# Optimization experiments

Hardware: AMD Instinct MI355X
Metric: run time of the kernel (lower is better)

## Reference

```python
import jax, jax.numpy as jnp
import numpy as np

HEADS, DQK, DV = 4, 128, 128
HH, WW = 32, 32
SCALE = DQK ** -0.5
EPS = 1e-5


def bn(x, g, b, m, v):
    # eval-mode BatchNorm2d over channel dim of NCHW
    inv = g * jax.lax.rsqrt(v + EPS)
    return x * inv[:, None, None] + (b - m * inv)[:, None, None]


def rel_to_abs(x):
    # x: (B, Nh, L, 2L-1) -> (B, Nh, L, L)
    B, Nh, L, _ = x.shape
    x = jnp.pad(x, ((0, 0), (0, 0), (0, 0), (0, 1)))
    fx = x.reshape(B, Nh, L * 2 * L)
    fx = jnp.pad(fx, ((0, 0), (0, 0), (0, L - 1)))
    fx = fx.reshape(B, Nh, L + 1, 2 * L - 1)
    return fx[:, :, :L, L - 1:]


def rel_logits_1d(q, rel_k):
    # q: (B, Nh, H, W, D); rel_k: (2W-1, D)
    B, Nh, H, W, D = q.shape
    r = jnp.einsum('bnhwd,rd->bnhwr', q, rel_k)
    r = rel_to_abs(r.reshape(B, Nh * H, W, 2 * W - 1))
    r = r.reshape(B, Nh, H, W, W)
    return jnp.broadcast_to(r[:, :, :, None], (B, Nh, H, H, W, W))


def pos_bias(q, rel_h, rel_w):
    # q: (B, Nh, H*W, D), already scaled
    B, Nh, L, D = q.shape
    q5 = q.reshape(B, Nh, HH, WW, D)
    rw = rel_logits_1d(q5, rel_w)                     # (B,N,H,Hx,W,W)
    rw = rw.transpose(0, 1, 2, 4, 3, 5).reshape(B, Nh, HH * WW, HH * WW)
    rh = rel_logits_1d(q5.transpose(0, 1, 3, 2, 4), rel_h)  # (B,N,W,Wx,H,H)
    rh = rh.transpose(0, 1, 4, 2, 5, 3).reshape(B, Nh, HH * WW, HH * WW)
    return rw + rh


def to_heads(x):
    # (B, Nh*d, H, W) -> (B, Nh, H*W, d)
    B, C, H, W = x.shape
    x = x.reshape(B, HEADS, C // HEADS, H, W)
    return x.transpose(0, 1, 3, 4, 2).reshape(B, HEADS, H * W, C // HEADS)


def mhsa(x, w_qk, w_v, rel_h, rel_w):
    B, C, H, W = x.shape
    qk = jnp.einsum('bchw,oc->bohw', x, w_qk)
    q, k = jnp.split(qk, 2, axis=1)
    v = jnp.einsum('bchw,oc->bohw', x, w_v)
    q, k, v = to_heads(q), to_heads(k), to_heads(v)
    q = q * SCALE
    logits = jnp.einsum('bnid,bnjd->bnij', q, k) + pos_bias(q, rel_h, rel_w)
    weights = jax.nn.softmax(logits, axis=-1)
    out = jnp.einsum('bnij,bnjd->bnid', weights, v)   # (B,Nh,HW,dv)
    out = out.reshape(B, HEADS, H, W, DV).transpose(0, 1, 4, 2, 3)
    return out.reshape(B, HEADS * DV, H, W)


def setup_inputs() -> dict:
    key = jax.random.key(0)
    ks = jax.random.split(key, 12)
    d = {
        'x': jax.random.normal(ks[0], (8, 512, HH, WW), jnp.float32),
        'w_qk': jax.random.normal(ks[1], (2 * HEADS * DQK, 512), jnp.float32) * 0.02,
        'w_v': jax.random.normal(ks[2], (HEADS * DV, 512), jnp.float32) * 0.02,
        'rel_h': jax.random.normal(ks[3], (2 * HH - 1, DQK), jnp.float32) * SCALE,
        'rel_w': jax.random.normal(ks[4], (2 * WW - 1, DQK), jnp.float32) * SCALE,
        'g1': jnp.ones((512,), jnp.float32),
        'b1': jnp.zeros((512,), jnp.float32),
        'm1': jax.random.normal(ks[5], (512,), jnp.float32) * 0.1,
        'v1': jax.random.uniform(ks[6], (512,), jnp.float32) + 0.5,
        'g2': jnp.ones((512,), jnp.float32),
        'b2': jnp.zeros((512,), jnp.float32),
        'm2': jax.random.normal(ks[7], (512,), jnp.float32) * 0.1,
        'v2': jax.random.uniform(ks[8], (512,), jnp.float32) + 0.5,
        'w_fc': jax.random.normal(ks[9], (512, 512, 3, 3), jnp.float32) * 0.02,
        'bias_fc': jnp.zeros((512,), jnp.float32),
    }
    return d


def reference(x, w_qk, w_v, rel_h, rel_w, g1, b1, m1, v1, g2, b2, m2, v2, w_fc, bias_fc):
    out = jax.nn.relu(bn(x, g1, b1, m1, v1))
    out = mhsa(out, w_qk, w_v, rel_h, rel_w)
    x = out + x
    out = jax.nn.relu(bn(x, g2, b2, m2, v2))
    out = jax.lax.conv_general_dilated(
        out, w_fc, window_strides=(1, 1), padding='SAME',
        dimension_numbers=('NCHW', 'OIHW', 'NCHW')) + bias_fc[:, None, None]
    return out + x
```

## Files before the change

kernel.cpp:

```cpp
#include <hip/hip_runtime.h>

typedef __bf16 v8bf __attribute__((ext_vector_type(8)));
typedef float f32x4 __attribute__((ext_vector_type(4)));

#define DEVI static __device__ __forceinline__

DEVI v8bf load8(const __bf16* p) { return *reinterpret_cast<const v8bf*>(p); }

DEVI f32x4 mfma16(v8bf a, v8bf b, f32x4 c) {
  return __builtin_amdgcn_mfma_f32_16x16x32_bf16(a, b, c, 0, 0, 0);
}

DEVI void gld16(const __bf16* g, __bf16* l) {
  __builtin_amdgcn_global_load_lds(
      (const __attribute__((address_space(1))) unsigned int*)(const void*)g,
      (__attribute__((address_space(3))) unsigned int*)(void*)l, 16, 0, 0);
}

#define SCALE_Q 0.08838834764831845f

__global__ void k_prep(const float* __restrict__ wqk, const float* __restrict__ wv,
                       const float* __restrict__ relh, const float* __restrict__ relw,
                       const float* __restrict__ wfc, __bf16* __restrict__ wqkb,
                       __bf16* __restrict__ wvb, __bf16* __restrict__ rhb,
                       __bf16* __restrict__ rwb, __bf16* __restrict__ Wt,
                       float* __restrict__ zpad4) {
  const int bid = blockIdx.x, tid = threadIdx.x;
  if (bid < 2048) {
    int i = bid * 256 + tid;
    wqkb[i] = (__bf16)wqk[i];
  } else if (bid < 3072) {
    int i = (bid - 2048) * 256 + tid;
    wvb[i] = (__bf16)wv[i];
  } else if (bid < 3104) {
    int i = (bid - 3072) * 256 + tid;
    if (i < 8064) rhb[i] = (__bf16)relh[i];
  } else if (bid < 3136) {
    int i = (bid - 3104) * 256 + tid;
    if (i < 8064) rwb[i] = (__bf16)relw[i];
  } else if (bid < 4160) {
    int i = (bid - 3136) * 256 + tid;
    const float* src = wfc + (size_t)i * 9;
#pragma unroll
    for (int tap = 0; tap < 9; ++tap)
      Wt[(size_t)tap * 262144 + i] = (__bf16)src[tap];
  } else {
    int i = (bid - 4160) * 256 + tid;
    f32x4 z = {0.f, 0.f, 0.f, 0.f};
    reinterpret_cast<f32x4*>(zpad4)[i] = z;
  }
}

__global__ void k_bn1(const float* __restrict__ x, const float* __restrict__ g,
                      const float* __restrict__ bb, const float* __restrict__ m,
                      const float* __restrict__ v, __bf16* __restrict__ y) {
  __shared__ float tile[32][33];
  const int b = blockIdx.z, c0 = blockIdx.y * 32, s0 = blockIdx.x * 32;
  const int tx = threadIdx.x, ty = threadIdx.y;
#pragma unroll
  for (int r = 0; r < 4; ++r) {
    int c = c0 + ty + r * 8;
    float inv = g[c] * rsqrtf(v[c] + 1e-5f);
    float beta = bb[c] - m[c] * inv;
    float val = x[((size_t)b * 512 + c) * 1024 + s0 + tx] * inv + beta;
    tile[ty + r * 8][tx] = fmaxf(val, 0.0f);
  }
  __syncthreads();
#pragma unroll
  for (int r = 0; r < 4; ++r) {
    int s = s0 + ty + r * 8;
    y[((size_t)b * 1024 + s) * 512 + c0 + tx] = (__bf16)tile[tx][ty + r * 8];
  }
}

__global__ void k_bn2(const float* __restrict__ x2, const float* __restrict__ g,
                      const float* __restrict__ bb, const float* __restrict__ m,
                      const float* __restrict__ v, __bf16* __restrict__ zp) {
  __shared__ float tile[32][33];
  const int b = blockIdx.z, c0 = blockIdx.y * 32, s0 = blockIdx.x * 32;
  const int tx = threadIdx.x, ty = threadIdx.y;
#pragma unroll
  for (int r = 0; r < 4; ++r) {
    int c = c0 + ty + r * 8;
    float inv = g[c] * rsqrtf(v[c] + 1e-5f);
    float beta = bb[c] - m[c] * inv;
    float val = x2[((size_t)b * 512 + c) * 1024 + s0 + tx] * inv + beta;
    tile[ty + r * 8][tx] = fmaxf(val, 0.0f);
  }
  __syncthreads();
#pragma unroll
  for (int r = 0; r < 4; ++r) {
    int s = s0 + ty + r * 8;
    int hh = s >> 5, ww = s & 31;
    zp[(((size_t)b * 34 + hh + 1) * 34 + ww + 1) * 512 + c0 + tx] =
        (__bf16)tile[tx][ty + r * 8];
  }
}

__global__ __launch_bounds__(256) void k_proj(
    const __bf16* __restrict__ wall, const __bf16* __restrict__ y,
    __bf16* __restrict__ qout, __bf16* __restrict__ kout,
    __bf16* __restrict__ vout) {
  __shared__ __bf16 As[128 * 32];
  __shared__ __bf16 Bs[128 * 32];
  const int t = threadIdx.x;
  const int wave = t >> 6, lane = t & 63;
  const int l15 = lane & 15, quad = lane >> 4;
  const int mbase = blockIdx.x * 128;
  const int nbase = blockIdx.y * 128;
  const int mh = (wave >> 1) * 64, nh = (wave & 1) * 64;
  const bool isv = mbase >= 1024;

  const int row0 = t >> 2, part8 = (t & 3) * 8;
  const __bf16* gA0 = wall + (size_t)(mbase + row0) * 512 + part8;
  const __bf16* gA1 = gA0 + (size_t)64 * 512;
  const __bf16* gB0 = y + (size_t)(nbase + row0) * 512 + part8;
  const __bf16* gB1 = gB0 + (size_t)64 * 512;
  __bf16* lA0 = As + (size_t)(wave * 64) * 8;
  __bf16* lA1 = As + (size_t)(256 + wave * 64) * 8;
  __bf16* lB0 = Bs + (size_t)(wave * 64) * 8;
  __bf16* lB1 = Bs + (size_t)(256 + wave * 64) * 8;

  const f32x4 fz = {0.f, 0.f, 0.f, 0.f};
  f32x4 acc[4][4];
#pragma unroll
  for (int i = 0; i < 4; ++i)
#pragma unroll
    for (int j = 0; j < 4; ++j) acc[i][j] = fz;

  for (int k0 = 0; k0 < 512; k0 += 32) {
    __syncthreads();
    gld16(gA0 + k0, lA0);
    gld16(gA1 + k0, lA1);
    gld16(gB0 + k0, lB0);
    gld16(gB1 + k0, lB1);
    __syncthreads();
    v8bf a[4], bfr[4];
#pragma unroll
    for (int i = 0; i < 4; ++i)
      a[i] = load8(&As[(size_t)(mh + i * 16 + l15) * 32 + quad * 8]);
#pragma unroll
    for (int j = 0; j < 4; ++j)
      bfr[j] = load8(&Bs[(size_t)(nh + j * 16 + l15) * 32 + quad * 8]);
    if (isv) {
#pragma unroll
      for (int i = 0; i < 4; ++i)
#pragma unroll
        for (int j = 0; j < 4; ++j) acc[i][j] = mfma16(a[i], bfr[j], acc[i][j]);
    } else {
#pragma unroll
      for (int i = 0; i < 4; ++i)
#pragma unroll
        for (int j = 0; j < 4; ++j) acc[i][j] = mfma16(bfr[j], a[i], acc[i][j]);
    }
  }

  if (isv) {
#pragma unroll
    for (int i = 0; i < 4; ++i)
#pragma unroll
      for (int j = 0; j < 4; ++j)
#pragma unroll
        for (int r = 0; r < 4; ++r) {
          int o = mbase + mh + i * 16 + quad * 4 + r;
          int nflat = nbase + nh + j * 16 + l15;
          int b = nflat >> 10, s = nflat & 1023;
          int oe = o - 1024; int n = oe >> 7, d = oe & 127;
          vout[(((size_t)b * 4 + n) * 128 + d) * 1024 + s] = (__bf16)acc[i][j][r];
        }
  } else {
    const bool isq = mbase < 512;
#pragma unroll
    for (int i = 0; i < 4; ++i)
#pragma unroll
      for (int j = 0; j < 4; ++j)
#pragma unroll
        for (int r = 0; r < 4; ++r) {
          int o = mbase + mh + i * 16 + l15;
          int nflat = nbase + nh + j * 16 + quad * 4 + r;
          int b = nflat >> 10, s = nflat & 1023;
          float val = acc[i][j][r];
          if (isq) {
            int n = o >> 7, d = o & 127;
            qout[(((size_t)b * 4 + n) * 1024 + s) * 128 + d] = (__bf16)(val * SCALE_Q);
          } else {
            int oe = o - 512; int n = oe >> 7, d = oe & 127;
            kout[(((size_t)b * 4 + n) * 1024 + s) * 128 + d] = (__bf16)val;
          }
        }
  }
}

__global__ __launch_bounds__(256, 2) void k_attn(
    const __bf16* __restrict__ q, const __bf16* __restrict__ kmat,
    const __bf16* __restrict__ vt, const __bf16* __restrict__ relh,
    const __bf16* __restrict__ relw, const float* __restrict__ x,
    float* __restrict__ x2) {
  __shared__ __bf16 Ks[2][4 * 64 * 32];
  __shared__ __bf16 Vs[2 * 128 * 32];
  __shared__ __bf16 P[4 * 16 * 68];
  __shared__ __bf16 RWs[64][33];
  __shared__ __bf16 RHs[64][33];
  __shared__ float Lt[4][16];

  const int Lb = blockIdx.x;
  const int xcd = Lb & 7, local = Lb >> 3;
  const int bn = xcd * 4 + (local & 3);
  const int qblk = local >> 2;
  const int s0 = qblk * 64;

  const int t = threadIdx.x;
  const int wave = t >> 6, lane = t & 63;
  const int l15 = lane & 15, quad = lane >> 4;
  const size_t hoff = ((size_t)bn) << 17;
  const int s0w = s0 + wave * 16;
  const int wlo = (wave & 1) * 16;
  const int h0w = s0w >> 5;

  const int row0 = t >> 2, part8 = (t & 3) * 8;
  const __bf16* kg = kmat + hoff + (size_t)row0 * 128 + part8;
  const __bf16* vg = vt + hoff + (size_t)row0 * 1024 + part8;
  __bf16* vsw = Vs + wave * 512;
  __bf16* ksw0 = Ks[0] + wave * 512;
  __bf16* ksw1 = Ks[1] + wave * 512;

#pragma unroll
  for (int kk2 = 0; kk2 < 2; ++kk2)
#pragma unroll
    for (int dh = 0; dh < 2; ++dh)
      gld16(vg + (size_t)dh * 64 * 1024 + kk2 * 32, vsw + kk2 * 4096 + dh * 2048);
#pragma unroll
  for (int kk = 0; kk < 4; ++kk)
    gld16(kg + kk * 32, ksw0 + kk * 2048);

  v8bf aq[4];
  {
    const __bf16* qp = q + hoff + (size_t)(s0w + l15) * 128;
#pragma unroll
    for (int kk = 0; kk < 4; ++kk) aq[kk] = load8(qp + kk * 32 + quad * 8);
  }

#pragma unroll
  for (int nt = 0; nt < 4; ++nt) {
    int rr = nt * 16 + l15;
    const __bf16* bp = relw + (size_t)rr * 128;
    f32x4 acc = {0.f, 0.f, 0.f, 0.f};
#pragma unroll
    for (int kk = 0; kk < 4; ++kk)
      acc = mfma16(aq[kk], load8(bp + kk * 32 + quad * 8), acc);
#pragma unroll
    for (int r = 0; r < 4; ++r) {
      int row = quad * 4 + r;
      int wj = rr + wlo + row - 31;
      if (wj >= 0 && wj < 32) RWs[wave * 16 + row][wj] = (__bf16)acc[r];
    }
  }
#pragma unroll
  for (int nt = 0; nt < 2; ++nt) {
    int hj = nt * 16 + l15;
    const __bf16* bp = relh + (size_t)(hj - h0w + 31) * 128;
    f32x4 acc = {0.f, 0.f, 0.f, 0.f};
#pragma unroll
    for (int kk = 0; kk < 4; ++kk)
      acc = mfma16(aq[kk], load8(bp + kk * 32 + quad * 8), acc);
#pragma unroll
    for (int r = 0; r < 4; ++r) RHs[wave * 16 + quad * 4 + r][hj] = (__bf16)acc[r];
  }

  __syncthreads();

  float rwreg[4][2];
#pragma unroll
  for (int r = 0; r < 4; ++r) {
    const int gi = wave * 16 + quad * 4 + r;
    rwreg[r][0] = (float)RWs[gi][l15];
    rwreg[r][1] = (float)RWs[gi][l15 + 16];
  }

  const f32x4 fz = {0.f, 0.f, 0.f, 0.f};
  float lsum[4] = {0.f, 0.f, 0.f, 0.f};
  f32x4 oacc[8];
#pragma unroll
  for (int dt = 0; dt < 8; ++dt) oacc[dt] = fz;
  __bf16* Pw = P + wave * 16 * 68;

#pragma unroll 1
  for (int iter = 0; iter < 16; ++iter) {
    const int cur = iter & 1;
    const __bf16* kcur = Ks[cur];
    __bf16* knxt = cur ? ksw0 : ksw1;
    const int jp = (iter < 15 ? iter + 1 : 15) * 64;

#pragma unroll
    for (int kk = 0; kk < 4; ++kk)
      gld16(kg + (size_t)jp * 128 + kk * 32, knxt + kk * 2048);

    f32x4 sacc[4];
    __builtin_amdgcn_s_setprio(1);
#pragma unroll
    for (int nj = 0; nj < 4; ++nj) {
      f32x4 a = fz;
#pragma unroll
      for (int kk = 0; kk < 4; ++kk)
        a = mfma16(aq[kk],
                   load8(&kcur[kk * 2048 + (nj * 16 + l15) * 32 + quad * 8]), a);
      sacc[nj] = a;
    }
    __builtin_amdgcn_s_setprio(0);

    const int hjb = iter * 2;
#pragma unroll
    for (int r = 0; r < 4; ++r) {
      const int row = quad * 4 + r;
      const int gi = wave * 16 + row;
      const float rw0 = rwreg[r][0], rw1 = rwreg[r][1];
      const float rh0 = (float)RHs[gi][hjb], rh1 = (float)RHs[gi][hjb + 1];
#pragma unroll
      for (int nj = 0; nj < 4; ++nj) {
        float val = sacc[nj][r] + ((nj & 1) ? rw1 : rw0) + ((nj & 2) ? rh1 : rh0);
        float p = __expf(fminf(val, 60.0f));
        lsum[r] += p;
        Pw[row * 68 + nj * 16 + l15] = (__bf16)p;
      }
    }
    v8bf pf[2];
#pragma unroll
    for (int kk2 = 0; kk2 < 2; ++kk2)
      pf[kk2] = *reinterpret_cast<const v8bf*>(&Pw[l15 * 68 + kk2 * 32 + quad * 8]);

    asm volatile("s_waitcnt vmcnt(4)" ::: "memory");
    __builtin_amdgcn_s_barrier();
    __builtin_amdgcn_sched_barrier(0);

    __builtin_amdgcn_s_setprio(1);
#pragma unroll
    for (int dt = 0; dt < 8; ++dt) {
      f32x4 a = oacc[dt];
#pragma unroll
      for (int kk2 = 0; kk2 < 2; ++kk2)
        a = mfma16(load8(&Vs[kk2 * 4096 + (dt * 16 + l15) * 32 + quad * 8]),
                   pf[kk2], a);
      oacc[dt] = a;
    }
    __builtin_amdgcn_s_setprio(0);

    __syncthreads();

#pragma unroll
    for (int kk2 = 0; kk2 < 2; ++kk2)
#pragma unroll
      for (int dh = 0; dh < 2; ++dh)
        gld16(vg + (size_t)dh * 64 * 1024 + jp + kk2 * 32,
              vsw + kk2 * 4096 + dh * 2048);
  }

#pragma unroll
  for (int r = 0; r < 4; ++r)
#pragma unroll
    for (int msk = 8; msk >= 1; msk >>= 1) lsum[r] += __shfl_xor(lsum[r], msk);
  if (l15 == 0) {
#pragma unroll
    for (int r = 0; r < 4; ++r) Lt[wave][quad * 4 + r] = lsum[r];
  }
  __syncthreads();

  {
    const float linv = 1.0f / Lt[wave][l15];
    const int s = s0w + l15;
#pragma unroll
    for (int dt = 0; dt < 8; ++dt)
#pragma unroll
      for (int r = 0; r < 4; ++r) {
        int d = dt * 16 + quad * 4 + r;
        size_t idx = ((size_t)bn * 128 + d) * 1024 + s;
        x2[idx] = oacc[dt][r] * linv + x[idx];
      }
  }
}

__global__ __launch_bounds__(256, 2) void k_conv(
    const __bf16* __restrict__ Wt, const __bf16* __restrict__ zp,
    float* __restrict__ part) {
  __shared__ __bf16 As[4 * 128 * 32];
  __shared__ __bf16 Bs[4 * 128 * 32];
  const int t = threadIdx.x;
  const int wave = t >> 6, lane = t & 63;
  const int l15 = lane & 15, quad = lane >> 4;

  const int id = blockIdx.x;
  const int combo = id & 7;
  const int ot = combo >> 1, sp = combo & 1;
  const int nt = id >> 3;
  const int mbase = ot * 128;
  const int nbase = nt * 128;
  const int cs = sp * 256;
  const int mh = (wave >> 1) * 64, nh = (wave & 1) * 64;

  const int row0 = t >> 2;
  const int part8 = (t & 3) * 8;
  const __bf16* gA0 = Wt + (size_t)(mbase + row0) * 512 + cs + part8;
  const __bf16* gA1 = gA0 + (size_t)64 * 512;
  const int n0 = nbase + row0;
  const int b0 = n0 >> 10, spn = n0 & 1023;
  const __bf16* gB0 =
      zp + ((size_t)(b0 * 34 + (spn >> 5) + 1) * 34 + (spn & 31) + 1) * 512 + cs + part8;
  const __bf16* gB1 = gB0 + (size_t)2 * 34 * 512;
  const int wofs = wave * 512;

  const f32x4 fz = {0.f, 0.f, 0.f, 0.f};
  f32x4 acc[4][4];
#pragma unroll
  for (int i = 0; i < 4; ++i)
#pragma unroll
    for (int j = 0; j < 4; ++j) acc[i][j] = fz;

#pragma unroll 1
  for (int tap = 0; tap < 9; ++tap) {
    const int dh = tap / 3 - 1, dw = tap % 3 - 1;
    const size_t aoff = (size_t)tap * 512 * 512;
    const int boff = (dh * 34 + dw) * 512;
#pragma unroll 1
    for (int k0 = 0; k0 < 256; k0 += 128) {
      __syncthreads();
#pragma unroll
      for (int c = 0; c < 4; ++c) {
        const int kq = k0 + c * 32;
        gld16(gA0 + aoff + kq, As + c * 4096 + wofs);
        gld16(gA1 + aoff + kq, As + c * 4096 + 2048 + wofs);
        gld16(gB0 + boff + kq, Bs + c * 4096 + wofs);
        gld16(gB1 + boff + kq, Bs + c * 4096 + 2048 + wofs);
      }
      __syncthreads();
#pragma unroll
      for (int c = 0; c < 4; ++c) {
        v8bf a[4], bfr[4];
#pragma unroll
        for (int i = 0; i < 4; ++i)
          a[i] = load8(&As[c * 4096 + (mh + i * 16 + l15) * 32 + quad * 8]);
#pragma unroll
        for (int j = 0; j < 4; ++j)
          bfr[j] = load8(&Bs[c * 4096 + (nh + j * 16 + l15) * 32 + quad * 8]);
#pragma unroll
        for (int i = 0; i < 4; ++i)
#pragma unroll
          for (int j = 0; j < 4; ++j) acc[i][j] = mfma16(a[i], bfr[j], acc[i][j]);
      }
    }
  }

  float* pout = part + (size_t)sp * 8 * 512 * 1024;
#pragma unroll
  for (int i = 0; i < 4; ++i)
#pragma unroll
    for (int j = 0; j < 4; ++j)
#pragma unroll
      for (int r = 0; r < 4; ++r) {
        int o = mbase + mh + i * 16 + quad * 4 + r;
        int nn = nbase + nh + j * 16 + l15;
        int bb2 = nn >> 10, s = nn & 1023;
        pout[((size_t)bb2 * 512 + o) * 1024 + s] = acc[i][j][r];
      }
}

__global__ void k_sum(const float* __restrict__ part, const float* __restrict__ bias,
                      const float* __restrict__ x2, float* __restrict__ out) {
  int i = blockIdx.x * 256 + threadIdx.x;
  int o = (i >> 8) & 511;
  f32x4 p0 = reinterpret_cast<const f32x4*>(part)[i];
  f32x4 p1 = reinterpret_cast<const f32x4*>(part + (size_t)8 * 512 * 1024)[i];
  f32x4 xr = reinterpret_cast<const f32x4*>(x2)[i];
  float bo = bias[o];
  f32x4 r;
#pragma unroll
  for (int c = 0; c < 4; ++c) r[c] = p0[c] + p1[c] + bo + xr[c];
  reinterpret_cast<f32x4*>(out)[i] = r;
}

extern "C" void kernel_launch(void* const* d_in, const int* in_sizes, int n_in,
                              void* d_out, int out_size, void* d_ws, size_t ws_size,
                              hipStream_t stream) {
  const float* x    = (const float*)d_in[0];
  const float* wqk  = (const float*)d_in[1];
  const float* wv   = (const float*)d_in[2];
  const float* relh = (const float*)d_in[3];
  const float* relw = (const float*)d_in[4];
  const float* g1   = (const float*)d_in[5];
  const float* b1   = (const float*)d_in[6];
  const float* m1   = (const float*)d_in[7];
  const float* v1   = (const float*)d_in[8];
  const float* g2   = (const float*)d_in[9];
  const float* b2   = (const float*)d_in[10];
  const float* m2   = (const float*)d_in[11];
  const float* v2   = (const float*)d_in[12];
  const float* wfc  = (const float*)d_in[13];
  const float* bfc  = (const float*)d_in[14];
  float* out = (float*)d_out;

  char* p = (char*)d_ws;
  __bf16* y    = (__bf16*)p; p += (size_t)8 * 1024 * 512 * 2;
  __bf16* qb   = (__bf16*)p; p += (size_t)8 * 4 * 1024 * 128 * 2;
  __bf16* kb   = (__bf16*)p; p += (size_t)8 * 4 * 1024 * 128 * 2;
  __bf16* vb   = (__bf16*)p; p += (size_t)8 * 4 * 1024 * 128 * 2;
  __bf16* Wt   = (__bf16*)p; p += (size_t)9 * 512 * 512 * 2;
  __bf16* wqkb = (__bf16*)p; p += (size_t)1024 * 512 * 2;
  __bf16* wvb  = (__bf16*)p; p += (size_t)512 * 512 * 2;
  __bf16* rhb  = (__bf16*)p; p += 32768;
  __bf16* rwb  = (__bf16*)p; p += 32768;
  float*  x2   = (float*)p;  p += (size_t)8 * 512 * 1024 * 4;
  __bf16* zpad = (__bf16*)p; p += (size_t)8 * 34 * 34 * 512 * 2;
  float* part = (float*)d_ws;

  k_prep<<<dim3(6472), dim3(256), 0, stream>>>(wqk, wv, relh, relw, wfc,
                                               wqkb, wvb, rhb, rwb, Wt, (float*)zpad);
  k_bn1<<<dim3(32, 16, 8), dim3(32, 8), 0, stream>>>(x, g1, b1, m1, v1, y);
  k_proj<<<dim3(12, 64), dim3(256), 0, stream>>>(wqkb, y, qb, kb, vb);
  k_attn<<<dim3(512), dim3(256), 0, stream>>>(qb, kb, vb, rhb, rwb, x, x2);
  k_bn2<<<dim3(32, 16, 8), dim3(32, 8), 0, stream>>>(x2, g2, b2, m2, v2, zpad);
  k_conv<<<dim3(512), dim3(256), 0, stream>>>(Wt, zpad, part);
  k_sum<<<dim3(4096), dim3(256), 0, stream>>>(part, bfc, x2, out);
}
```

Measured before the change: 238.8 us.

## Split attention key range across two blocks and merge partials in BN2 kernel

Attention work is split along the key dimension into two halves, doubling the grid to 1024 blocks. Each block writes an unnormalized partial output and partial row sums, and the BN2 kernel combines them, normalizes, and adds the residual. This is possible without a running max because softmax uses a clamped exponent. K is no longer double-buffered, which frees LDS for three blocks per CU, but each iteration now waits on its loads with an extra barrier. The change adds extra global traffic for the two fp32 partial outputs.

```diff
diff --git a/kernel.cpp b/kernel.cpp
--- a/kernel.cpp
+++ b/kernel.cpp
@@ -73,19 +73,27 @@
   }
 }
 
-__global__ void k_bn2(const float* __restrict__ x2, const float* __restrict__ g,
-                      const float* __restrict__ bb, const float* __restrict__ m,
-                      const float* __restrict__ v, __bf16* __restrict__ zp) {
+__global__ void k_bn2c(float* o0x2, const float* __restrict__ o1,
+                       const float* __restrict__ lp, const float* __restrict__ xin,
+                       const float* __restrict__ g, const float* __restrict__ bb,
+                       const float* __restrict__ m, const float* __restrict__ v,
+                       __bf16* __restrict__ zp) {
   __shared__ float tile[32][33];
   const int b = blockIdx.z, c0 = blockIdx.y * 32, s0 = blockIdx.x * 32;
   const int tx = threadIdx.x, ty = threadIdx.y;
+  const int bnrow = b * 4 + (c0 >> 7);
+  const int scol = s0 + tx;
+  const float linv =
+      1.0f / (lp[bnrow * 1024 + scol] + lp[32768 + bnrow * 1024 + scol]);
 #pragma unroll
   for (int r = 0; r < 4; ++r) {
     int c = c0 + ty + r * 8;
     float inv = g[c] * rsqrtf(v[c] + 1e-5f);
     float beta = bb[c] - m[c] * inv;
-    float val = x2[((size_t)b * 512 + c) * 1024 + s0 + tx] * inv + beta;
-    tile[ty + r * 8][tx] = fmaxf(val, 0.0f);
+    size_t idx = ((size_t)b * 512 + c) * 1024 + scol;
+    float t = (o0x2[idx] + o1[idx]) * linv + xin[idx];
+    o0x2[idx] = t;
+    tile[ty + r * 8][tx] = fmaxf(t * inv + beta, 0.0f);
   }
   __syncthreads();
 #pragma unroll
@@ -191,22 +199,22 @@
   }
 }
 
-__global__ __launch_bounds__(256, 2) void k_attn(
+__global__ __launch_bounds__(256, 3) void k_attn(
     const __bf16* __restrict__ q, const __bf16* __restrict__ kmat,
     const __bf16* __restrict__ vt, const __bf16* __restrict__ relh,
-    const __bf16* __restrict__ relw, const float* __restrict__ x,
-    float* __restrict__ x2) {
-  __shared__ __bf16 Ks[2][4 * 64 * 32];
+    const __bf16* __restrict__ relw, float* __restrict__ o0,
+    float* __restrict__ o1, float* __restrict__ lpart) {
+  __shared__ __bf16 Ks[4 * 64 * 32];
   __shared__ __bf16 Vs[2 * 128 * 32];
   __shared__ __bf16 P[4 * 16 * 68];
   __shared__ __bf16 RWs[64][33];
   __shared__ __bf16 RHs[64][33];
-  __shared__ float Lt[4][16];
 
   const int Lb = blockIdx.x;
   const int xcd = Lb & 7, local = Lb >> 3;
   const int bn = xcd * 4 + (local & 3);
-  const int qblk = local >> 2;
+  const int qblk = (local >> 2) & 15;
+  const int half = local >> 6;
   const int s0 = qblk * 64;
 
   const int t = threadIdx.x;
@@ -220,18 +228,19 @@
   const int row0 = t >> 2, part8 = (t & 3) * 8;
   const __bf16* kg = kmat + hoff + (size_t)row0 * 128 + part8;
   const __bf16* vg = vt + hoff + (size_t)row0 * 1024 + part8;
+  __bf16* ksw = Ks + wave * 512;
   __bf16* vsw = Vs + wave * 512;
-  __bf16* ksw0 = Ks[0] + wave * 512;
-  __bf16* ksw1 = Ks[1] + wave * 512;
-
+
+  const int j00 = half * 512;
+#pragma unroll
+  for (int kk = 0; kk < 4; ++kk)
+    gld16(kg + (size_t)j00 * 128 + kk * 32, ksw + kk * 2048);
 #pragma unroll
   for (int kk2 = 0; kk2 < 2; ++kk2)
 #pragma unroll
     for (int dh = 0; dh < 2; ++dh)
-      gld16(vg + (size_t)dh * 64 * 1024 + kk2 * 32, vsw + kk2 * 4096 + dh * 2048);
-#pragma unroll
-  for (int kk = 0; kk < 4; ++kk)
-    gld16(kg + kk * 32, ksw0 + kk * 2048);
+      gld16(vg + (size_t)dh * 64 * 1024 + j00 + kk2 * 32,
+            vsw + kk2 * 4096 + dh * 2048);
 
   v8bf aq[4];
   {
@@ -285,16 +294,7 @@
   __bf16* Pw = P + wave * 16 * 68;
 
 #pragma unroll 1
-  for (int iter = 0; iter < 16; ++iter) {
-    const int cur = iter & 1;
-    const __bf16* kcur = Ks[cur];
-    __bf16* knxt = cur ? ksw0 : ksw1;
-    const int jp = (iter < 15 ? iter + 1 : 15) * 64;
-
-#pragma unroll
-    for (int kk = 0; kk < 4; ++kk)
-      gld16(kg + (size_t)jp * 128 + kk * 32, knxt + kk * 2048);
-
+  for (int iter = 0; iter < 8; ++iter) {
     f32x4 sacc[4];
     __builtin_amdgcn_s_setprio(1);
 #pragma unroll
@@ -303,12 +303,12 @@
 #pragma unroll
       for (int kk = 0; kk < 4; ++kk)
         a = mfma16(aq[kk],
-                   load8(&kcur[kk * 2048 + (nj * 16 + l15) * 32 + quad * 8]), a);
+                   load8(&Ks[kk * 2048 + (nj * 16 + l15) * 32 + quad * 8]), a);
       sacc[nj] = a;
     }
     __builtin_amdgcn_s_setprio(0);
 
-    const int hjb = iter * 2;
+    const int hjb = half * 16 + iter * 2;
 #pragma unroll
     for (int r = 0; r < 4; ++r) {
       const int row = quad * 4 + r;
@@ -328,7 +328,7 @@
     for (int kk2 = 0; kk2 < 2; ++kk2)
       pf[kk2] = *reinterpret_cast<const v8bf*>(&Pw[l15 * 68 + kk2 * 32 + quad * 8]);
 
-    asm volatile("s_waitcnt vmcnt(4)" ::: "memory");
+    asm volatile("s_waitcnt vmcnt(0)" ::: "memory");
     __builtin_amdgcn_s_barrier();
     __builtin_amdgcn_sched_barrier(0);
 
@@ -346,12 +346,21 @@
 
     __syncthreads();
 
-#pragma unroll
-    for (int kk2 = 0; kk2 < 2; ++kk2)
-#pragma unroll
-      for (int dh = 0; dh < 2; ++dh)
-        gld16(vg + (size_t)dh * 64 * 1024 + jp + kk2 * 32,
-              vsw + kk2 * 4096 + dh * 2048);
+    if (iter < 7) {
+      const int jn = j00 + (iter + 1) * 64;
+#pragma unroll
+      for (int kk = 0; kk < 4; ++kk)
+        gld16(kg + (size_t)jn * 128 + kk * 32, ksw + kk * 2048);
+#pragma unroll
+      for (int kk2 = 0; kk2 < 2; ++kk2)
+#pragma unroll
+        for (int dh = 0; dh < 2; ++dh)
+          gld16(vg + (size_t)dh * 64 * 1024 + jn + kk2 * 32,
+                vsw + kk2 * 4096 + dh * 2048);
+      asm volatile("s_waitcnt vmcnt(4)" ::: "memory");
+      __builtin_amdgcn_s_barrier();
+      __builtin_amdgcn_sched_barrier(0);
+    }
   }
 
 #pragma unroll
@@ -360,20 +369,19 @@
     for (int msk = 8; msk >= 1; msk >>= 1) lsum[r] += __shfl_xor(lsum[r], msk);
   if (l15 == 0) {
 #pragma unroll
-    for (int r = 0; r < 4; ++r) Lt[wave][quad * 4 + r] = lsum[r];
-  }
-  __syncthreads();
+    for (int r = 0; r < 4; ++r)
+      lpart[half * 32768 + bn * 1024 + s0w + quad * 4 + r] = lsum[r];
+  }
 
   {
-    const float linv = 1.0f / Lt[wave][l15];
+    float* op = half ? o1 : o0;
     const int s = s0w + l15;
 #pragma unroll
     for (int dt = 0; dt < 8; ++dt)
 #pragma unroll
       for (int r = 0; r < 4; ++r) {
         int d = dt * 16 + quad * 4 + r;
-        size_t idx = ((size_t)bn * 128 + d) * 1024 + s;
-        x2[idx] = oacc[dt][r] * linv + x[idx];
+        op[((size_t)bn * 128 + d) * 1024 + s] = oacc[dt][r];
       }
   }
 }
@@ -508,14 +516,18 @@
   __bf16* rwb  = (__bf16*)p; p += 32768;
   float*  x2   = (float*)p;  p += (size_t)8 * 512 * 1024 * 4;
   __bf16* zpad = (__bf16*)p; p += (size_t)8 * 34 * 34 * 512 * 2;
+  float* lpart = (float*)d_ws;
+  float* o0 = x2;
+  float* o1 = (float*)d_out;
   float* part = (float*)d_ws;
 
   k_prep<<<dim3(6472), dim3(256), 0, stream>>>(wqk, wv, relh, relw, wfc,
                                                wqkb, wvb, rhb, rwb, Wt, (float*)zpad);
   k_bn1<<<dim3(32, 16, 8), dim3(32, 8), 0, stream>>>(x, g1, b1, m1, v1, y);
   k_proj<<<dim3(12, 64), dim3(256), 0, stream>>>(wqkb, y, qb, kb, vb);
-  k_attn<<<dim3(512), dim3(256), 0, stream>>>(qb, kb, vb, rhb, rwb, x, x2);
-  k_bn2<<<dim3(32, 16, 8), dim3(32, 8), 0, stream>>>(x2, g2, b2, m2, v2, zpad);
+  k_attn<<<dim3(1024), dim3(256), 0, stream>>>(qb, kb, vb, rhb, rwb, o0, o1, lpart);
+  k_bn2c<<<dim3(32, 16, 8), dim3(32, 8), 0, stream>>>(o0, o1, lpart, x,
+                                                      g2, b2, m2, v2, zpad);
   k_conv<<<dim3(512), dim3(256), 0, stream>>>(Wt, zpad, part);
   k_sum<<<dim3(4096), dim3(256), 0, stream>>>(part, bfc, x2, out);
 }
```

Result: slower. 252.7 us (+5.8%).
